# Optimization experiments

Hardware: AMD Instinct MI355X
Metric: run time of the kernel (lower is better)

The kernel has to match this reference:

```python
import jax, jax.numpy as jnp
import numpy as np

B, C, H, W = 8, 256, 128, 128
K = 5            # k_up
GROUPS = 32      # min(C, 32)
EPS = 1e-5       # BatchNorm eps


def _conv2d(x, w, b, pad=0, groups=1):
    out = jax.lax.conv_general_dilated(
        x, w, window_strides=(1, 1), padding=[(pad, pad), (pad, pad)],
        dimension_numbers=('NCHW', 'OIHW', 'NCHW'), feature_group_count=groups)
    return out + b[None, :, None, None]


def _bn(x, g, b, m, v):
    # inference-mode BatchNorm2d
    inv = jax.lax.rsqrt(v + EPS)
    return (x - m[None, :, None, None]) * (g * inv)[None, :, None, None] + b[None, :, None, None]


def setup_inputs() -> dict:
    key = jax.random.key(0)
    ks = jax.random.split(key, 12)
    s3 = 1.0 / np.sqrt(9 * C / GROUPS)
    s3d = 1.0 / np.sqrt(9 * C)
    s1 = 1.0 / np.sqrt(C)
    return {
        'x': jax.random.normal(ks[0], (B, C, H, W), jnp.float32),
        # kernel_enc: grouped 3x3 conv -> BN -> SiLU -> 1x1 conv -> softmax
        'ke_w1': jax.random.normal(ks[1], (C, C // GROUPS, 3, 3), jnp.float32) * s3,
        'ke_b1': jnp.zeros((C,), jnp.float32),
        'ke_bn_g': jnp.ones((C,), jnp.float32),
        'ke_bn_b': jnp.zeros((C,), jnp.float32),
        'ke_bn_m': jax.random.normal(ks[2], (C,), jnp.float32) * 0.1,
        'ke_bn_v': jax.random.uniform(ks[3], (C,), jnp.float32, 0.5, 1.5),
        'ke_w2': jax.random.normal(ks[4], (K * K, C, 1, 1), jnp.float32) * s1,
        'ke_b2': jnp.zeros((K * K,), jnp.float32),
        # blend_static: dense 3x3 conv -> BN -> SiLU
        'bs_w': jax.random.normal(ks[5], (C, C, 3, 3), jnp.float32) * s3d,
        'bs_b': jnp.zeros((C,), jnp.float32),
        'bs_bn_g': jnp.ones((C,), jnp.float32),
        'bs_bn_b': jnp.zeros((C,), jnp.float32),
        'bs_bn_m': jax.random.normal(ks[6], (C,), jnp.float32) * 0.1,
        'bs_bn_v': jax.random.uniform(ks[7], (C,), jnp.float32, 0.5, 1.5),
        # gate: GAP -> 1x1 conv -> sigmoid
        'g_w': jax.random.normal(ks[8], (1, C, 1, 1), jnp.float32) * s1,
        'g_b': jnp.zeros((1,), jnp.float32),
    }


def _apply_carafe(x, kernels):
    # x: [B,C,H,W], kernels: [B,K*K,H,W] (softmax over kernel dim)
    pad = K // 2
    x_pad = jnp.pad(x, ((0, 0), (0, 0), (pad, pad), (pad, pad)), mode='reflect')
    out = jnp.zeros_like(x)
    # fixed K*K=25 taps; flatten order (ki over H, kj over W) matches torch unfold
    for n in range(K * K):
        ki, kj = n // K, n % K
        out = out + x_pad[:, :, ki:ki + H, kj:kj + W] * kernels[:, n][:, None]
    return out


def reference(x, ke_w1, ke_b1, ke_bn_g, ke_bn_b, ke_bn_m, ke_bn_v, ke_w2, ke_b2,
              bs_w, bs_b, bs_bn_g, bs_bn_b, bs_bn_m, bs_bn_v, g_w, g_b):
    # static branch
    static = jax.nn.silu(_bn(_conv2d(x, bs_w, bs_b, pad=1), bs_bn_g, bs_bn_b, bs_bn_m, bs_bn_v))
    # dynamic kernels
    h = jax.nn.silu(_bn(_conv2d(x, ke_w1, ke_b1, pad=1, groups=GROUPS), ke_bn_g, ke_bn_b, ke_bn_m, ke_bn_v))
    kernels = jax.nn.softmax(_conv2d(h, ke_w2, ke_b2), axis=1)  # [B,K*K,H,W]
    carafe = _apply_carafe(x, kernels)
    # channel-agnostic global gate
    g = jax.nn.sigmoid(_conv2d(jnp.mean(x, axis=(2, 3), keepdims=True), g_w, g_b))  # [B,1,1,1]
    return g * carafe + (1.0 - g) * static
```

## Files before the change

### kernel.cpp

```cpp
#include <hip/hip_runtime.h>

#define EPS_ 1e-5f

typedef __attribute__((ext_vector_type(8))) short bf16x8;
typedef __attribute__((ext_vector_type(8))) unsigned short u16x8;
typedef __attribute__((ext_vector_type(4))) unsigned short u16x4;
typedef __attribute__((ext_vector_type(4))) float f32x4;
typedef __attribute__((ext_vector_type(2))) float f32x2;
typedef __attribute__((ext_vector_type(2))) unsigned int u32x2;
typedef __attribute__((address_space(3))) u16x8 lds_u16x8;
typedef __attribute__((address_space(3))) f32x4 lds_f32x4;
typedef __attribute__((address_space(3))) u32x2 lds_u32x2;
typedef __attribute__((address_space(3))) bf16x8 lds_bf16x8;

__device__ __forceinline__ float sigmoidf_(float v) { return 1.f / (1.f + __expf(-v)); }

__device__ __forceinline__ unsigned short f2bf(float f) {
  unsigned int u = __float_as_uint(f);
  u += 0x7fff + ((u >> 16) & 1);
  return (unsigned short)(u >> 16);
}

__device__ __forceinline__ float bf2f(unsigned short u) {
  return __uint_as_float((unsigned int)u << 16);
}

__device__ __forceinline__ f32x2 pkfma_(f32x2 a, f32x2 b, f32x2 c) {
#if __has_builtin(__builtin_elementwise_fma)
  return __builtin_elementwise_fma(a, b, c);
#else
  return (f32x2){fmaf(a.x, b.x, c.x), fmaf(a.y, b.y, c.y)};
#endif
}

__device__ __forceinline__ void gload16(const void* g, void* l) {
  __builtin_amdgcn_global_load_lds((const __attribute__((address_space(1))) unsigned int*)(g),
                                   (__attribute__((address_space(3))) unsigned int*)(l), 16, 0, 0);
}

__global__ void gate_kernel(const float* __restrict__ partial, const float* __restrict__ gw,
                            const float* __restrict__ gb, float* __restrict__ gout) {
  int b = blockIdx.x, t = threadIdx.x;
  float s = partial[b * 256 + t] * gw[t];
#pragma unroll
  for (int off = 32; off; off >>= 1) s += __shfl_down(s, off, 64);
  __shared__ float red[4];
  if ((t & 63) == 0) red[t >> 6] = s;
  __syncthreads();
  if (t == 0) {
    float tot = (red[0] + red[1]) + (red[2] + red[3]);
    gout[b] = sigmoidf_(tot * (1.f / 16384.f) + gb[0]);
  }
}

__global__ void prep_kernel(const float* __restrict__ w, unsigned short* __restrict__ wT,
                            const float* __restrict__ w1, const float* __restrict__ b1,
                            const float* __restrict__ bng, const float* __restrict__ bnb,
                            const float* __restrict__ bnm, const float* __restrict__ bnv,
                            const float* __restrict__ w2, const float* __restrict__ b2,
                            unsigned short* __restrict__ w1b, unsigned short* __restrict__ w2b,
                            float* __restrict__ b1f, float* __restrict__ b2p,
                            float* __restrict__ zb) {
  int blk = blockIdx.x;
  if (blk < 2304) {
    int n = blk * 256 + threadIdx.x;
    int c = n & 31, oc = (n >> 5) & 255, t9 = n >> 13;
    int cb = t9 / 9, tap = t9 - cb * 9;
    wT[n] = f2bf(w[(oc * 256 + cb * 32 + c) * 9 + tap]);
  } else if (blk < 2464) {
    int n = (blk - 2304) * 256 + threadIdx.x;
    int j = n & 7, r1 = n >> 3;
    int lane = r1 & 63, r2 = r1 >> 6;
    int step = r2 % 5, gp = r2 / 5;
    int oc_l = lane & 15, kg2 = lane >> 4;
    int k = step * 32 + kg2 * 8 + j;
    int tap = k >> 4, icp = k & 15;
    int c = gp * 16 + oc_l;
    bool valid = (tap < 9) && ((icp >> 3) == (oc_l >> 3));
    float s = bng[c] * rsqrtf(bnv[c] + EPS_);
    w1b[n] = f2bf(valid ? w1[c * 72 + (icp & 7) * 9 + tap] * s : 0.f);
  } else if (blk < 2496) {
    int n = (blk - 2464) * 256 + threadIdx.x;
    int j = n & 7, r1 = n >> 3;
    int lane = r1 & 63, r2 = r1 >> 6;
    int ntile = r2 & 1, rnd = r2 >> 1;
    int nn = ntile * 16 + (lane & 15);
    int c = rnd * 32 + (lane >> 4) * 8 + j;
    w2b[n] = f2bf((nn < 25) ? w2[nn * 256 + c] : 0.f);
  } else {
    int n = threadIdx.x;
    if (n < 16) zb[n] = 0.f;
    if (n < 32) b2p[n] = (n < 25) ? b2[n] : -1e30f;
    if (n < 256) {
      float s = bng[n] * rsqrtf(bnv[n] + EPS_);
      b1f[n] = (b1[n] - bnm[n]) * s + bnb[n];
    }
  }
}

__global__ __launch_bounds__(256) void transpose_kernel(const float* __restrict__ x,
                                                        unsigned short* __restrict__ xT,
                                                        float* __restrict__ partial) {
  int blk = blockIdx.x;
  int tile = blk & 255, b = blk >> 8;
  int px0 = tile * 64;
  __shared__ unsigned int tr[64 * 130];
  for (int i = threadIdx.x; i < 1024; i += 256) {
    int ch2 = i >> 3, pc = i & 7;
    const float* p0 = x + (((size_t)b * 256 + ch2 * 2) << 14) + px0 + pc * 8;
    const float4* a4 = (const float4*)p0;
    const float4* b4 = (const float4*)(p0 + 16384);
    float4 a0 = a4[0], a1 = a4[1], b0 = b4[0], b1 = b4[1];
    float fa[8] = {a0.x, a0.y, a0.z, a0.w, a1.x, a1.y, a1.z, a1.w};
    float fb[8] = {b0.x, b0.y, b0.z, b0.w, b1.x, b1.y, b1.z, b1.w};
    float sa = 0.f, sb = 0.f;
#pragma unroll
    for (int j = 0; j < 8; ++j) {
      sa += fa[j];
      sb += fb[j];
      unsigned int w = (unsigned int)f2bf(fa[j]) | ((unsigned int)f2bf(fb[j]) << 16);
      tr[(pc * 8 + j) * 130 + ch2] = w;
    }
    sa += __shfl_down(sa, 4, 8); sa += __shfl_down(sa, 2, 8); sa += __shfl_down(sa, 1, 8);
    sb += __shfl_down(sb, 4, 8); sb += __shfl_down(sb, 2, 8); sb += __shfl_down(sb, 1, 8);
    if ((threadIdx.x & 7) == 0) {
      atomicAdd(&partial[(b << 8) + ch2 * 2], sa);
      atomicAdd(&partial[(b << 8) + ch2 * 2 + 1], sb);
    }
  }
  __syncthreads();
  for (int i = threadIdx.x; i < 2048; i += 256) {
    int px = i >> 5, kc = i & 31;
    uint4 v = *(uint4*)&tr[px * 130 + kc * 4];
    *(uint4*)(xT + ((((size_t)b << 14)) + px0 + px) * 256 + kc * 8) = v;
  }
}

__device__ __forceinline__ void kernelgen_body(
    int kblk, const unsigned short* __restrict__ xT, const unsigned short* __restrict__ w1b,
    const unsigned short* __restrict__ w2b, const float* __restrict__ b1f,
    const float* __restrict__ b2p, const unsigned short* __restrict__ zbuf,
    float* __restrict__ kern, char* smemc) {
  char* hbufc = smemc + 10368;
  int t = kblk & 63, b = kblk >> 6;
  int px0 = (t & 7) * 16, py0 = (t >> 3) * 16;
  int lane = threadIdx.x & 63, wid = threadIdx.x >> 6;
  int nx = lane & 15, kgrp = lane >> 4;
  const char* zc = (const char*)zbuf;

  size_t soff[3];
  bool okk[3];
#pragma unroll
  for (int i = 0; i < 3; ++i) {
    int g = wid * 162 + i * 64 + lane;
    int p = g >> 1, half = g & 1;
    int hy = p / 18, hx = p - hy * 18;
    int gy = py0 + hy - 1, gx = px0 + hx - 1;
    okk[i] = ((unsigned)gy < 128u) && ((unsigned)gx < 128u);
    soff[i] = (size_t)((gy & 127) * 128 + (gx & 127)) * 512 + half * 16;
  }
  const char* imgbase = (const char*)xT + (((size_t)b << 14) * 512);
  int dstb = wid * 2592;

  int aoff[5];
  int base_t = nx * 32 + (kgrp & 1) * 16;
#pragma unroll
  for (int s = 0; s < 5; ++s) {
    int tap = 2 * s + (kgrp >> 1);
    if (tap > 8) tap = 8;
    int dy = tap / 3, dx = tap - dy * 3;
    aoff[s] = dy * 576 + dx * 32 + base_t;
  }

  f32x4 acc2[4][2];
#pragma unroll
  for (int ml = 0; ml < 4; ++ml)
#pragma unroll
    for (int nt = 0; nt < 2; ++nt) acc2[ml][nt] = (f32x4)0.f;

#pragma unroll 1
  for (int gp = 0; gp < 16; ++gp) {
    __syncthreads();
    gload16(okk[0] ? imgbase + soff[0] + gp * 32 : zc, smemc + dstb);
    gload16(okk[1] ? imgbase + soff[1] + gp * 32 : zc, smemc + dstb + 1024);
    if (lane < 34) gload16(okk[2] ? imgbase + soff[2] + gp * 32 : zc, smemc + dstb + 2048);
    asm volatile("s_waitcnt vmcnt(0)" ::: "memory");
    __builtin_amdgcn_s_barrier();
    asm volatile("" ::: "memory");

    bf16x8 wf[5];
    const unsigned short* wp = w1b + ((size_t)(gp * 5) * 64 + lane) * 8;
#pragma unroll
    for (int s = 0; s < 5; ++s) wf[s] = *(const bf16x8*)(wp + s * 512);
    f32x4 bias = *(const f32x4*)(b1f + gp * 16 + kgrp * 4);

#pragma unroll
    for (int ml = 0; ml < 4; ++ml) {
      int m = wid * 4 + ml;
      f32x4 cf = (f32x4)0.f;
#pragma unroll
      for (int s = 0; s < 5; ++s) {
        bf16x8 xf = *(lds_bf16x8*)(smemc + m * 576 + aoff[s]);
        cf = __builtin_amdgcn_mfma_f32_16x16x32_bf16(wf[s], xf, cf, 0, 0, 0);
      }
      unsigned short us[4];
#pragma unroll
      for (int r = 0; r < 4; ++r) {
        float hv = cf[r] + bias[r];
        us[r] = f2bf(hv * sigmoidf_(hv));
      }
      unsigned int lo = (unsigned int)us[0] | ((unsigned int)us[1] << 16);
      unsigned int hi = (unsigned int)us[2] | ((unsigned int)us[3] << 16);
      *(lds_u32x2*)(hbufc + (m * 16 + nx) * 80 + (gp & 1) * 32 + kgrp * 8) = (u32x2){lo, hi};
    }

    if (gp & 1) {
      int rnd = gp >> 1;
      const unsigned short* w2p = w2b + ((size_t)(rnd * 2) * 64 + lane) * 8;
      bf16x8 w2f0 = *(const bf16x8*)(w2p);
      bf16x8 w2f1 = *(const bf16x8*)(w2p + 512);
#pragma unroll
      for (int ml = 0; ml < 4; ++ml) {
        int m = wid * 4 + ml;
        bf16x8 hf = *(lds_bf16x8*)(hbufc + (m * 16 + nx) * 80 + kgrp * 16);
        acc2[ml][0] = __builtin_amdgcn_mfma_f32_16x16x32_bf16(w2f0, hf, acc2[ml][0], 0, 0, 0);
        acc2[ml][1] = __builtin_amdgcn_mfma_f32_16x16x32_bf16(w2f1, hf, acc2[ml][1], 0, 0, 0);
      }
    }
  }

  f32x4 blo = *(const f32x4*)(b2p + kgrp * 4);
  f32x4 bhi = *(const f32x4*)(b2p + 16 + kgrp * 4);
#pragma unroll
  for (int ml = 0; ml < 4; ++ml) {
    int m = wid * 4 + ml;
    float v[8];
#pragma unroll
    for (int r = 0; r < 4; ++r) {
      v[r] = acc2[ml][0][r] + blo[r];
      v[4 + r] = acc2[ml][1][r] + bhi[r];
    }
    float mx = v[0];
#pragma unroll
    for (int i = 1; i < 8; ++i) mx = fmaxf(mx, v[i]);
    mx = fmaxf(mx, __shfl_xor(mx, 16, 64));
    mx = fmaxf(mx, __shfl_xor(mx, 32, 64));
    float sum = 0.f;
#pragma unroll
    for (int i = 0; i < 8; ++i) { v[i] = __expf(v[i] - mx); sum += v[i]; }
    sum += __shfl_xor(sum, 16, 64);
    sum += __shfl_xor(sum, 32, 64);
    float inv = 1.f / sum;
    size_t base = (((size_t)b * 25) << 14) + (size_t)(py0 + m) * 128 + px0 + nx;
#pragma unroll
    for (int nt = 0; nt < 2; ++nt)
#pragma unroll
      for (int r = 0; r < 4; ++r) {
        int n = nt * 16 + kgrp * 4 + r;
        if (n < 25) kern[base + ((size_t)n << 14)] = v[nt * 4 + r] * inv;
      }
  }
}

__device__ __forceinline__ void conv_body(int cblk, const unsigned short* __restrict__ xT,
                                          const unsigned short* __restrict__ wT,
                                          const float* __restrict__ bb,
                                          const float* __restrict__ bng,
                                          const float* __restrict__ bnb,
                                          const float* __restrict__ bnm,
                                          const float* __restrict__ bnv,
                                          const unsigned short* __restrict__ zbuf,
                                          unsigned short* __restrict__ statb,
                                          float* __restrict__ out, char* smemc) {
  int nb = ((cblk & 7) << 8) | (cblk >> 3);
  int ocb = nb & 1, y = (nb >> 1) & 127, b = nb >> 8;
  int lane = threadIdx.x & 63, wid = threadIdx.x >> 6;
  int m_l = lane & 15, kgrp = lane >> 4;

  unsigned short* xs = (unsigned short*)smemc;
  const char* zc = (const char*)zbuf;

  int g0 = wid * 130 + lane, g1 = g0 + 64, g2 = wid * 130 + 128 + lane;
  int px0_ = g0 >> 2, k0_ = g0 & 3, s0_ = k0_ ^ ((px0_ >> 1) & 3), gx0 = px0_ - 1;
  int px1_ = g1 >> 2, k1_ = g1 & 3, s1_ = k1_ ^ ((px1_ >> 1) & 3), gx1 = px1_ - 1;
  int px2_ = g2 >> 2, k2_ = g2 & 3, s2_ = k2_ ^ ((px2_ >> 1) & 3), gx2 = px2_ - 1;
  bool ok0 = (unsigned)gx0 < 128u, ok1 = (unsigned)gx1 < 128u, ok2 = (unsigned)gx2 < 128u;
  int off0 = gx0 * 512 + s0_ * 16, off1 = gx1 * 512 + s1_ * 16, off2 = gx2 * 512 + s2_ * 16;
  int d0 = (wid * 130) * 16, d1 = d0 + 1024, d2 = d0 + 2048;

#define STAGE_ROW(slotB_, cbn_, khn_)                                                       \
  do {                                                                                      \
    int gy_ = y + (khn_)-1;                                                                 \
    bool gyok_ = ((unsigned)gy_ < 128u);                                                    \
    const char* rb_ =                                                                       \
        (const char*)xT + (((size_t)b << 14) + (size_t)(gy_ & 127) * 128) * 512 + (cbn_)*64;\
    gload16((gyok_ && ok0) ? rb_ + off0 : zc, smemc + (slotB_) + d0);                       \
    gload16((gyok_ && ok1) ? rb_ + off1 : zc, smemc + (slotB_) + d1);                       \
    if (lane < 2) gload16((gyok_ && ok2) ? rb_ + off2 : zc, smemc + (slotB_) + d2);         \
  } while (0)

  f32x4 acc[8][2];
#pragma unroll
  for (int mt = 0; mt < 8; ++mt)
#pragma unroll
    for (int nt = 0; nt < 2; ++nt) acc[mt][nt] = (f32x4)0.f;

  STAGE_ROW(0, 0, 0);
  STAGE_ROW(8320, 0, 1);
  STAGE_ROW(16640, 0, 2);
  STAGE_ROW(24960, 1, 0);

  int oc0 = ocb * 128 + wid * 32;
  const unsigned short* wTb = wT + ((size_t)(oc0 + m_l) * 32 + kgrp * 8);
  int khn = 1, cbn = 1;

#pragma unroll 1
  for (int P = 0; P < 12; ++P) {
    if (P < 11) {
      asm volatile("s_waitcnt vmcnt(6)" ::: "memory");
    } else {
      asm volatile("s_waitcnt vmcnt(0)" ::: "memory");
    }
    __builtin_amdgcn_s_barrier();
    asm volatile("" ::: "memory");
#pragma unroll
    for (int half = 0; half < 2; ++half) {
      int R = 2 * P + half;
      const unsigned short* xb = xs + (R & 3) * 4160;
#pragma unroll
      for (int kw = 0; kw < 3; ++kw) {
        bf16x8 bfrag[2];
        const unsigned short* wb = wTb + (size_t)(R * 3 + kw) * 8192;
#pragma unroll
        for (int nt = 0; nt < 2; ++nt) bfrag[nt] = *(const bf16x8*)(wb + nt * 512);
#pragma unroll
        for (int mt = 0; mt < 8; ++mt) {
          int apx = mt * 16 + m_l + kw;
          int kk = kgrp ^ ((apx >> 1) & 3);
          bf16x8 af =
              *(__attribute__((address_space(3))) bf16x8*)(&xb[apx * 32 + kk * 8]);
#pragma unroll
          for (int nt = 0; nt < 2; ++nt)
            acc[mt][nt] =
                __builtin_amdgcn_mfma_f32_16x16x32_bf16(af, bfrag[nt], acc[mt][nt], 0, 0, 0);
        }
      }
    }
    __builtin_amdgcn_s_barrier();
    asm volatile("" ::: "memory");
    if (P < 10) {
      STAGE_ROW((size_t)((2 * P + 4) & 3) * 8320, cbn, khn);
      ++khn;
      if (khn == 3) { khn = 0; ++cbn; }
      STAGE_ROW((size_t)((2 * P + 5) & 3) * 8320, cbn, khn);
      ++khn;
      if (khn == 3) { khn = 0; ++cbn; }
    }
  }
#undef STAGE_ROW

  float scale2[2], bias2[2];
#pragma unroll
  for (int nt = 0; nt < 2; ++nt) {
    int oc = oc0 + nt * 16 + m_l;
    float s = bng[oc] * rsqrtf(bnv[oc] + EPS_);
    scale2[nt] = s;
    bias2[nt] = bnb[oc] + (bb[oc] - bnm[oc]) * s;
  }
  if (statb) {
#pragma unroll
    for (int nt = 0; nt < 2; ++nt) {
      size_t obase = (((size_t)(b * 256 + oc0 + nt * 16 + m_l)) << 14) + y * 128 + kgrp * 4;
#pragma unroll
      for (int mt = 0; mt < 8; ++mt) {
        f32x4 v = acc[mt][nt];
        u16x4 o;
#pragma unroll
        for (int r = 0; r < 4; ++r) {
          float hv = v[r] * scale2[nt] + bias2[nt];
          o[r] = f2bf(hv * sigmoidf_(hv));
        }
        *(u16x4*)(statb + obase + mt * 16) = o;
      }
    }
  } else {
#pragma unroll
    for (int nt = 0; nt < 2; ++nt) {
      size_t obase = (((size_t)(b * 256 + oc0 + nt * 16 + m_l)) << 14) + y * 128 + kgrp * 4;
#pragma unroll
      for (int mt = 0; mt < 8; ++mt) {
        f32x4 v = acc[mt][nt];
        float o4[4];
#pragma unroll
        for (int r = 0; r < 4; ++r) {
          float hv = v[r] * scale2[nt] + bias2[nt];
          o4[r] = hv * sigmoidf_(hv);
        }
        *(f32x4*)(out + obase + mt * 16) = (f32x4){o4[0], o4[1], o4[2], o4[3]};
      }
    }
  }
}

__global__ __launch_bounds__(256, 4) void fused_kernel(
    int kgN, const unsigned short* __restrict__ xT, const unsigned short* __restrict__ wT,
    const unsigned short* __restrict__ w1b, const unsigned short* __restrict__ w2b,
    const float* __restrict__ b1f, const float* __restrict__ b2p, float* __restrict__ kern,
    const float* __restrict__ bb, const float* __restrict__ bng, const float* __restrict__ bnb,
    const float* __restrict__ bnm, const float* __restrict__ bnv,
    const unsigned short* __restrict__ zbuf, unsigned short* __restrict__ statb,
    float* __restrict__ out) {
  __shared__ char smem[33280];
  int blk = (int)blockIdx.x;
  if (blk < kgN) {
    kernelgen_body(blk, xT, w1b, w2b, b1f, b2p, zbuf, kern, smem);
  } else {
    conv_body(blk - kgN, xT, wT, bb, bng, bnb, bnm, bnv, zbuf, statb, out, smem);
  }
}

__global__ __launch_bounds__(256) void carafe_blend_kernel(
    const unsigned short* __restrict__ xT, const float* __restrict__ kern,
    const float* __restrict__ gq, const unsigned short* __restrict__ statb,
    float* __restrict__ out) {
  int blk = blockIdx.x;
  int xcd = blk & 7, r = blk >> 3;
  int ocg = r & 15;
  int tile = (r >> 4) * 8 + xcd;
  int b = tile >> 5, rem = tile & 31;
  int by = rem >> 3, bx = rem & 7;
  __shared__ unsigned short xc[720 * 16];
  int lane = threadIdx.x & 63, wid = threadIdx.x >> 6;
  int lx = threadIdx.x & 15, y0 = (threadIdx.x >> 4) * 2;
  float gv = gq[b];
  int gy0 = by * 32 + y0, gx = bx * 16 + lx;

  float kv0[25], kv1[25];
  size_t kb = (((size_t)b * 25) << 14) + gy0 * 128 + gx;
#pragma unroll
  for (int n = 0; n < 25; ++n) {
    kv0[n] = kern[kb + ((size_t)n << 14)];
    kv1[n] = kern[kb + ((size_t)n << 14) + 128];
  }

  int dstb = wid * 5760;
#pragma unroll
  for (int i = 0; i < 6; ++i) {
    int g = wid * 360 + i * 64 + lane;
    if (i < 5 || lane < 40) {
      int p = g >> 1, half = g & 1;
      int py = p / 20, pxx = p - py * 20;
      int yy = by * 32 + py - 2, xx = bx * 16 + pxx - 2;
      yy = yy < 0 ? -yy : (yy > 127 ? 254 - yy : yy);
      xx = xx < 0 ? -xx : (xx > 127 ? 254 - xx : xx);
      gload16((const char*)xT + ((size_t)((b << 14) + yy * 128 + xx) * 512) + ocg * 32 +
                  half * 16,
              (char*)xc + dstb + i * 1024);
    }
  }
  asm volatile("s_waitcnt vmcnt(0)" ::: "memory");
  __syncthreads();

  f32x2 car0[8], car1[8];
#pragma unroll
  for (int c = 0; c < 8; ++c) { car0[c] = (f32x2)0.f; car1[c] = (f32x2)0.f; }
#pragma unroll
  for (int n = 0; n < 25; ++n) {
    int ki = n / 5, kj = n - ki * 5;
    int p0 = (y0 + ki) * 20 + lx + kj;
    f32x2 kvv0 = (f32x2){kv0[n], kv0[n]}, kvv1 = (f32x2){kv1[n], kv1[n]};
    union { u16x8 s8; unsigned int u[4]; } a0, a1, b0, b1;
    a0.s8 = *(lds_u16x8*)(&xc[p0 * 16]);
    a1.s8 = *(lds_u16x8*)(&xc[p0 * 16 + 8]);
    b0.s8 = *(lds_u16x8*)(&xc[(p0 + 20) * 16]);
    b1.s8 = *(lds_u16x8*)(&xc[(p0 + 20) * 16 + 8]);
#pragma unroll
    for (int j = 0; j < 4; ++j) {
      f32x2 f0 = (f32x2){__uint_as_float(a0.u[j] << 16), __uint_as_float(a0.u[j] & 0xffff0000u)};
      f32x2 f1 = (f32x2){__uint_as_float(a1.u[j] << 16), __uint_as_float(a1.u[j] & 0xffff0000u)};
      f32x2 g0 = (f32x2){__uint_as_float(b0.u[j] << 16), __uint_as_float(b0.u[j] & 0xffff0000u)};
      f32x2 g1 = (f32x2){__uint_as_float(b1.u[j] << 16), __uint_as_float(b1.u[j] & 0xffff0000u)};
      car0[j] = pkfma_(f0, kvv0, car0[j]);
      car0[4 + j] = pkfma_(f1, kvv0, car0[4 + j]);
      car1[j] = pkfma_(g0, kvv1, car1[j]);
      car1[4 + j] = pkfma_(g1, kvv1, car1[4 + j]);
    }
  }
  if (statb) {
#pragma unroll
    for (int j = 0; j < 8; ++j) {
      size_t ob0 = (((size_t)(b * 256 + ocg * 16 + 2 * j)) << 14) + gy0 * 128 + gx;
      size_t ob1 = ob0 + 16384;
      float s00 = bf2f(statb[ob0]), s01 = bf2f(statb[ob0 + 128]);
      float s10 = bf2f(statb[ob1]), s11 = bf2f(statb[ob1 + 128]);
      out[ob0] = fmaf(gv, car0[j].x - s00, s00);
      out[ob0 + 128] = fmaf(gv, car1[j].x - s01, s01);
      out[ob1] = fmaf(gv, car0[j].y - s10, s10);
      out[ob1 + 128] = fmaf(gv, car1[j].y - s11, s11);
    }
  } else {
#pragma unroll
    for (int j = 0; j < 8; ++j) {
      size_t ob0 = (((size_t)(b * 256 + ocg * 16 + 2 * j)) << 14) + gy0 * 128 + gx;
      size_t ob1 = ob0 + 16384;
      float s00 = out[ob0], s01 = out[ob0 + 128];
      float s10 = out[ob1], s11 = out[ob1 + 128];
      out[ob0] = fmaf(gv, car0[j].x - s00, s00);
      out[ob0 + 128] = fmaf(gv, car1[j].x - s01, s01);
      out[ob1] = fmaf(gv, car0[j].y - s10, s10);
      out[ob1 + 128] = fmaf(gv, car1[j].y - s11, s11);
    }
  }
}

extern "C" void kernel_launch(void* const* d_in, const int* in_sizes, int n_in,
                              void* d_out, int out_size, void* d_ws, size_t ws_size,
                              hipStream_t stream) {
  const float* x      = (const float*)d_in[0];
  const float* ke_w1  = (const float*)d_in[1];
  const float* ke_b1  = (const float*)d_in[2];
  const float* ke_bng = (const float*)d_in[3];
  const float* ke_bnb = (const float*)d_in[4];
  const float* ke_bnm = (const float*)d_in[5];
  const float* ke_bnv = (const float*)d_in[6];
  const float* ke_w2  = (const float*)d_in[7];
  const float* ke_b2  = (const float*)d_in[8];
  const float* bs_w   = (const float*)d_in[9];
  const float* bs_b   = (const float*)d_in[10];
  const float* bs_bng = (const float*)d_in[11];
  const float* bs_bnb = (const float*)d_in[12];
  const float* bs_bnm = (const float*)d_in[13];
  const float* bs_bnv = (const float*)d_in[14];
  const float* g_w    = (const float*)d_in[15];
  const float* g_b    = (const float*)d_in[16];
  float* outp = (float*)d_out;

  char* ws = (char*)d_ws;
  float* kern        = (float*)(ws);
  float* partial     = (float*)(ws + 13107200);
  float* gout        = (float*)(ws + 13115392);
  float* zbuff       = (float*)(ws + 13115392 + 128);
  unsigned short* wT = (unsigned short*)(ws + 13115648);
  unsigned short* xT = (unsigned short*)(ws + 14295296);

  const size_t USED = 81404160;
  const size_t TBL = 131072;
  bool bigws = ws_size >= USED + TBL;
  bool bigws2 = ws_size >= USED + TBL + 67108864;
  unsigned short *w1b, *w2b;
  float *b1f, *b2p;
  if (bigws) {
    w1b = (unsigned short*)(ws + USED);
    w2b = (unsigned short*)(ws + USED + 81920);
    b1f = (float*)(ws + USED + 98304);
    b2p = (float*)(ws + USED + 99328);
  } else {
    w1b = (unsigned short*)((char*)d_out + 52428800);
    w2b = (unsigned short*)((char*)d_out + 52428800 + 81920);
    b1f = (float*)((char*)d_out + 52428800 + 98304);
    b2p = (float*)((char*)d_out + 52428800 + 99328);
  }
  unsigned short* statb = bigws2 ? (unsigned short*)(ws + USED + TBL) : nullptr;

  hipMemsetAsync(partial, 0, 2048 * sizeof(float), stream);
  prep_kernel<<<2497, 256, 0, stream>>>(bs_w, wT, ke_w1, ke_b1, ke_bng, ke_bnb, ke_bnm,
                                        ke_bnv, ke_w2, ke_b2, w1b, w2b, b1f, b2p, zbuff);
  transpose_kernel<<<2048, 256, 0, stream>>>(x, xT, partial);
  gate_kernel<<<8, 256, 0, stream>>>(partial, g_w, g_b, gout);

  if (bigws) {
    fused_kernel<<<2560, 256, 0, stream>>>(512, xT, wT, w1b, w2b, b1f, b2p, kern, bs_b,
                                           bs_bng, bs_bnb, bs_bnm, bs_bnv,
                                           (const unsigned short*)zbuff, statb, outp);
  } else {
    fused_kernel<<<512, 256, 0, stream>>>(512, xT, wT, w1b, w2b, b1f, b2p, kern, bs_b,
                                          bs_bng, bs_bnb, bs_bnm, bs_bnv,
                                          (const unsigned short*)zbuff, statb, outp);
    fused_kernel<<<2048, 256, 0, stream>>>(0, xT, wT, w1b, w2b, b1f, b2p, kern, bs_b,
                                           bs_bng, bs_bnb, bs_bnm, bs_bnv,
                                           (const unsigned short*)zbuff, statb, outp);
  }
  carafe_blend_kernel<<<4096, 256, 0, stream>>>(xT, kern, gout, statb, outp);
}
```

Baseline: 510.3 us.

## Merge prep/transpose and gate into existing launches; reshape carafe tile to 32x16

```diff
diff --git a/kernel.cpp b/kernel.cpp
--- a/kernel.cpp
+++ b/kernel.cpp
@@ -38,30 +38,51 @@
                                    (__attribute__((address_space(3))) unsigned int*)(l), 16, 0, 0);
 }
 
-__global__ void gate_kernel(const float* __restrict__ partial, const float* __restrict__ gw,
-                            const float* __restrict__ gb, float* __restrict__ gout) {
-  int b = blockIdx.x, t = threadIdx.x;
-  float s = partial[b * 256 + t] * gw[t];
-#pragma unroll
-  for (int off = 32; off; off >>= 1) s += __shfl_down(s, off, 64);
-  __shared__ float red[4];
-  if ((t & 63) == 0) red[t >> 6] = s;
-  __syncthreads();
-  if (t == 0) {
-    float tot = (red[0] + red[1]) + (red[2] + red[3]);
-    gout[b] = sigmoidf_(tot * (1.f / 16384.f) + gb[0]);
-  }
-}
-
-__global__ void prep_kernel(const float* __restrict__ w, unsigned short* __restrict__ wT,
-                            const float* __restrict__ w1, const float* __restrict__ b1,
-                            const float* __restrict__ bng, const float* __restrict__ bnb,
-                            const float* __restrict__ bnm, const float* __restrict__ bnv,
-                            const float* __restrict__ w2, const float* __restrict__ b2,
-                            unsigned short* __restrict__ w1b, unsigned short* __restrict__ w2b,
-                            float* __restrict__ b1f, float* __restrict__ b2p,
-                            float* __restrict__ zb) {
-  int blk = blockIdx.x;
+__global__ __launch_bounds__(256) void prep_transpose_kernel(
+    const float* __restrict__ x, unsigned short* __restrict__ xT, float* __restrict__ partial,
+    const float* __restrict__ w, unsigned short* __restrict__ wT,
+    const float* __restrict__ w1, const float* __restrict__ b1, const float* __restrict__ bng,
+    const float* __restrict__ bnb, const float* __restrict__ bnm, const float* __restrict__ bnv,
+    const float* __restrict__ w2, const float* __restrict__ b2,
+    unsigned short* __restrict__ w1b, unsigned short* __restrict__ w2b,
+    float* __restrict__ b1f, float* __restrict__ b2p, float* __restrict__ zb) {
+  __shared__ unsigned int tr[64 * 130];
+  int ablk = blockIdx.x;
+  if (ablk < 2048) {
+    int tile = ablk & 255, b = ablk >> 8;
+    int px0 = tile * 64;
+    for (int i = threadIdx.x; i < 1024; i += 256) {
+      int ch2 = i >> 3, pc = i & 7;
+      const float* p0 = x + (((size_t)b * 256 + ch2 * 2) << 14) + px0 + pc * 8;
+      const float4* a4 = (const float4*)p0;
+      const float4* b4 = (const float4*)(p0 + 16384);
+      float4 a0 = a4[0], a1 = a4[1], b0 = b4[0], b1v = b4[1];
+      float fa[8] = {a0.x, a0.y, a0.z, a0.w, a1.x, a1.y, a1.z, a1.w};
+      float fb[8] = {b0.x, b0.y, b0.z, b0.w, b1v.x, b1v.y, b1v.z, b1v.w};
+      float sa = 0.f, sb = 0.f;
+#pragma unroll
+      for (int j = 0; j < 8; ++j) {
+        sa += fa[j];
+        sb += fb[j];
+        unsigned int wv = (unsigned int)f2bf(fa[j]) | ((unsigned int)f2bf(fb[j]) << 16);
+        tr[(pc * 8 + j) * 130 + ch2] = wv;
+      }
+      sa += __shfl_down(sa, 4, 8); sa += __shfl_down(sa, 2, 8); sa += __shfl_down(sa, 1, 8);
+      sb += __shfl_down(sb, 4, 8); sb += __shfl_down(sb, 2, 8); sb += __shfl_down(sb, 1, 8);
+      if ((threadIdx.x & 7) == 0) {
+        atomicAdd(&partial[(b << 8) + ch2 * 2], sa);
+        atomicAdd(&partial[(b << 8) + ch2 * 2 + 1], sb);
+      }
+    }
+    __syncthreads();
+    for (int i = threadIdx.x; i < 2048; i += 256) {
+      int px = i >> 5, kc = i & 31;
+      uint4 v = *(uint4*)&tr[px * 130 + kc * 4];
+      *(uint4*)(xT + ((((size_t)b << 14)) + px0 + px) * 256 + kc * 8) = v;
+    }
+    return;
+  }
+  int blk = ablk - 2048;
   if (blk < 2304) {
     int n = blk * 256 + threadIdx.x;
     int c = n & 31, oc = (n >> 5) & 255, t9 = n >> 13;
@@ -98,44 +119,6 @@
   }
 }
 
-__global__ __launch_bounds__(256) void transpose_kernel(const float* __restrict__ x,
-                                                        unsigned short* __restrict__ xT,
-                                                        float* __restrict__ partial) {
-  int blk = blockIdx.x;
-  int tile = blk & 255, b = blk >> 8;
-  int px0 = tile * 64;
-  __shared__ unsigned int tr[64 * 130];
-  for (int i = threadIdx.x; i < 1024; i += 256) {
-    int ch2 = i >> 3, pc = i & 7;
-    const float* p0 = x + (((size_t)b * 256 + ch2 * 2) << 14) + px0 + pc * 8;
-    const float4* a4 = (const float4*)p0;
-    const float4* b4 = (const float4*)(p0 + 16384);
-    float4 a0 = a4[0], a1 = a4[1], b0 = b4[0], b1 = b4[1];
-    float fa[8] = {a0.x, a0.y, a0.z, a0.w, a1.x, a1.y, a1.z, a1.w};
-    float fb[8] = {b0.x, b0.y, b0.z, b0.w, b1.x, b1.y, b1.z, b1.w};
-    float sa = 0.f, sb = 0.f;
-#pragma unroll
-    for (int j = 0; j < 8; ++j) {
-      sa += fa[j];
-      sb += fb[j];
-      unsigned int w = (unsigned int)f2bf(fa[j]) | ((unsigned int)f2bf(fb[j]) << 16);
-      tr[(pc * 8 + j) * 130 + ch2] = w;
-    }
-    sa += __shfl_down(sa, 4, 8); sa += __shfl_down(sa, 2, 8); sa += __shfl_down(sa, 1, 8);
-    sb += __shfl_down(sb, 4, 8); sb += __shfl_down(sb, 2, 8); sb += __shfl_down(sb, 1, 8);
-    if ((threadIdx.x & 7) == 0) {
-      atomicAdd(&partial[(b << 8) + ch2 * 2], sa);
-      atomicAdd(&partial[(b << 8) + ch2 * 2 + 1], sb);
-    }
-  }
-  __syncthreads();
-  for (int i = threadIdx.x; i < 2048; i += 256) {
-    int px = i >> 5, kc = i & 31;
-    uint4 v = *(uint4*)&tr[px * 130 + kc * 4];
-    *(uint4*)(xT + ((((size_t)b << 14)) + px0 + px) * 256 + kc * 8) = v;
-  }
-}
-
 __device__ __forceinline__ void kernelgen_body(
     int kblk, const unsigned short* __restrict__ xT, const unsigned short* __restrict__ w1b,
     const unsigned short* __restrict__ w2b, const float* __restrict__ b1f,
@@ -402,6 +385,23 @@
   }
 }
 
+__device__ __forceinline__ void gate_body(int b, const float* __restrict__ partial,
+                                          const float* __restrict__ gw,
+                                          const float* __restrict__ gb,
+                                          float* __restrict__ gout, char* smemc) {
+  float* red = (float*)smemc;
+  int t = threadIdx.x;
+  float s = partial[b * 256 + t] * gw[t];
+#pragma unroll
+  for (int off = 32; off; off >>= 1) s += __shfl_down(s, off, 64);
+  if ((t & 63) == 0) red[t >> 6] = s;
+  __syncthreads();
+  if (t == 0) {
+    float tot = (red[0] + red[1]) + (red[2] + red[3]);
+    gout[b] = sigmoidf_(tot * (1.f / 16384.f) + gb[0]);
+  }
+}
+
 __global__ __launch_bounds__(256, 4) void fused_kernel(
     int kgN, const unsigned short* __restrict__ xT, const unsigned short* __restrict__ wT,
     const unsigned short* __restrict__ w1b, const unsigned short* __restrict__ w2b,
@@ -409,13 +409,16 @@
     const float* __restrict__ bb, const float* __restrict__ bng, const float* __restrict__ bnb,
     const float* __restrict__ bnm, const float* __restrict__ bnv,
     const unsigned short* __restrict__ zbuf, unsigned short* __restrict__ statb,
-    float* __restrict__ out) {
+    float* __restrict__ out, const float* __restrict__ partial, const float* __restrict__ gw,
+    const float* __restrict__ gb, float* __restrict__ gout) {
   __shared__ char smem[33280];
   int blk = (int)blockIdx.x;
   if (blk < kgN) {
     kernelgen_body(blk, xT, w1b, w2b, b1f, b2p, zbuf, kern, smem);
+  } else if (blk < kgN + 2048) {
+    conv_body(blk - kgN, xT, wT, bb, bng, bnb, bnm, bnv, zbuf, statb, out, smem);
   } else {
-    conv_body(blk - kgN, xT, wT, bb, bng, bnb, bnm, bnv, zbuf, statb, out, smem);
+    gate_body(blk - kgN - 2048, partial, gw, gb, gout, smem);
   }
 }
 
@@ -428,15 +431,16 @@
   int ocg = r & 15;
   int tile = (r >> 4) * 8 + xcd;
   int b = tile >> 5, rem = tile & 31;
-  int by = rem >> 3, bx = rem & 7;
+  int by = rem >> 2, bx = rem & 3;
   __shared__ unsigned short xc[720 * 16];
   int lane = threadIdx.x & 63, wid = threadIdx.x >> 6;
-  int lx = threadIdx.x & 15, y0 = (threadIdx.x >> 4) * 2;
+  int lx = threadIdx.x & 31, ty = threadIdx.x >> 5;
   float gv = gq[b];
-  int gy0 = by * 32 + y0, gx = bx * 16 + lx;
+  int y0 = ty * 2;
+  int gy0 = by * 16 + y0, gx = bx * 32 + lx;
 
   float kv0[25], kv1[25];
-  size_t kb = (((size_t)b * 25) << 14) + gy0 * 128 + gx;
+  size_t kb = (((size_t)b * 25) << 14) + (size_t)gy0 * 128 + gx;
 #pragma unroll
   for (int n = 0; n < 25; ++n) {
     kv0[n] = kern[kb + ((size_t)n << 14)];
@@ -449,8 +453,8 @@
     int g = wid * 360 + i * 64 + lane;
     if (i < 5 || lane < 40) {
       int p = g >> 1, half = g & 1;
-      int py = p / 20, pxx = p - py * 20;
-      int yy = by * 32 + py - 2, xx = bx * 16 + pxx - 2;
+      int py = p / 36, pxx = p - py * 36;
+      int yy = by * 16 + py - 2, xx = bx * 32 + pxx - 2;
       yy = yy < 0 ? -yy : (yy > 127 ? 254 - yy : yy);
       xx = xx < 0 ? -xx : (xx > 127 ? 254 - xx : xx);
       gload16((const char*)xT + ((size_t)((b << 14) + yy * 128 + xx) * 512) + ocg * 32 +
@@ -467,13 +471,13 @@
 #pragma unroll
   for (int n = 0; n < 25; ++n) {
     int ki = n / 5, kj = n - ki * 5;
-    int p0 = (y0 + ki) * 20 + lx + kj;
+    int p0 = (y0 + ki) * 36 + lx + kj;
     f32x2 kvv0 = (f32x2){kv0[n], kv0[n]}, kvv1 = (f32x2){kv1[n], kv1[n]};
     union { u16x8 s8; unsigned int u[4]; } a0, a1, b0, b1;
     a0.s8 = *(lds_u16x8*)(&xc[p0 * 16]);
     a1.s8 = *(lds_u16x8*)(&xc[p0 * 16 + 8]);
-    b0.s8 = *(lds_u16x8*)(&xc[(p0 + 20) * 16]);
-    b1.s8 = *(lds_u16x8*)(&xc[(p0 + 20) * 16 + 8]);
+    b0.s8 = *(lds_u16x8*)(&xc[(p0 + 36) * 16]);
+    b1.s8 = *(lds_u16x8*)(&xc[(p0 + 36) * 16 + 8]);
 #pragma unroll
     for (int j = 0; j < 4; ++j) {
       f32x2 f0 = (f32x2){__uint_as_float(a0.u[j] << 16), __uint_as_float(a0.u[j] & 0xffff0000u)};
@@ -489,7 +493,7 @@
   if (statb) {
 #pragma unroll
     for (int j = 0; j < 8; ++j) {
-      size_t ob0 = (((size_t)(b * 256 + ocg * 16 + 2 * j)) << 14) + gy0 * 128 + gx;
+      size_t ob0 = (((size_t)(b * 256 + ocg * 16 + 2 * j)) << 14) + (size_t)gy0 * 128 + gx;
       size_t ob1 = ob0 + 16384;
       float s00 = bf2f(statb[ob0]), s01 = bf2f(statb[ob0 + 128]);
       float s10 = bf2f(statb[ob1]), s11 = bf2f(statb[ob1 + 128]);
@@ -501,7 +505,7 @@
   } else {
 #pragma unroll
     for (int j = 0; j < 8; ++j) {
-      size_t ob0 = (((size_t)(b * 256 + ocg * 16 + 2 * j)) << 14) + gy0 * 128 + gx;
+      size_t ob0 = (((size_t)(b * 256 + ocg * 16 + 2 * j)) << 14) + (size_t)gy0 * 128 + gx;
       size_t ob1 = ob0 + 16384;
       float s00 = out[ob0], s01 = out[ob0 + 128];
       float s10 = out[ob1], s11 = out[ob1 + 128];
@@ -563,22 +567,23 @@
   unsigned short* statb = bigws2 ? (unsigned short*)(ws + USED + TBL) : nullptr;
 
   hipMemsetAsync(partial, 0, 2048 * sizeof(float), stream);
-  prep_kernel<<<2497, 256, 0, stream>>>(bs_w, wT, ke_w1, ke_b1, ke_bng, ke_bnb, ke_bnm,
-                                        ke_bnv, ke_w2, ke_b2, w1b, w2b, b1f, b2p, zbuff);
-  transpose_kernel<<<2048, 256, 0, stream>>>(x, xT, partial);
-  gate_kernel<<<8, 256, 0, stream>>>(partial, g_w, g_b, gout);
-
+  prep_transpose_kernel<<<4545, 256, 0, stream>>>(x, xT, partial, bs_w, wT, ke_w1, ke_b1,
+                                                  ke_bng, ke_bnb, ke_bnm, ke_bnv, ke_w2,
+                                                  ke_b2, w1b, w2b, b1f, b2p, zbuff);
   if (bigws) {
-    fused_kernel<<<2560, 256, 0, stream>>>(512, xT, wT, w1b, w2b, b1f, b2p, kern, bs_b,
+    fused_kernel<<<2568, 256, 0, stream>>>(512, xT, wT, w1b, w2b, b1f, b2p, kern, bs_b,
                                            bs_bng, bs_bnb, bs_bnm, bs_bnv,
-                                           (const unsigned short*)zbuff, statb, outp);
+                                           (const unsigned short*)zbuff, statb, outp,
+                                           partial, g_w, g_b, gout);
   } else {
     fused_kernel<<<512, 256, 0, stream>>>(512, xT, wT, w1b, w2b, b1f, b2p, kern, bs_b,
                                           bs_bng, bs_bnb, bs_bnm, bs_bnv,
-                                          (const unsigned short*)zbuff, statb, outp);
-    fused_kernel<<<2048, 256, 0, stream>>>(0, xT, wT, w1b, w2b, b1f, b2p, kern, bs_b,
+                                          (const unsigned short*)zbuff, statb, outp,
+                                          partial, g_w, g_b, gout);
+    fused_kernel<<<2056, 256, 0, stream>>>(0, xT, wT, w1b, w2b, b1f, b2p, kern, bs_b,
                                            bs_bng, bs_bnb, bs_bnm, bs_bnv,
-                                           (const unsigned short*)zbuff, statb, outp);
+                                           (const unsigned short*)zbuff, statb, outp,
+                                           partial, g_w, g_b, gout);
   }
   carafe_blend_kernel<<<4096, 256, 0, stream>>>(xT, kern, gout, statb, outp);
 }
```

Measured after the change: 476.2 us. 1.07x faster.
